# Kernel optimization log

Measured on AMD Instinct MI355X. Metric: run time of the kernel, lower is better.

The kernel has to match this reference:

```python
import jax, jax.numpy as jnp
import numpy as np

DIM = 512
NH, NKV, HD = 8, 4, DIM // 8
KVD = NKV * HD
EPS = 1.1920928955078125e-07  # torch.finfo(float32).eps (F.rms_norm default)
ROPE_BASE = 10000.0


def _rms_norm(x):
    # F.rms_norm over last dim, no learned weight
    ms = jnp.mean(jnp.square(x), axis=-1, keepdims=True)
    return x * jax.lax.rsqrt(ms + EPS)


def _rope_tables(T, dtype):
    inv_freq = 1.0 / (ROPE_BASE ** (jnp.arange(0, HD, 2, dtype=jnp.float32) / HD))
    t = jnp.arange(T, dtype=jnp.float32)
    f = jnp.outer(t, inv_freq)  # [T, HD//2]
    return jnp.cos(f).astype(dtype)[None, None], jnp.sin(f).astype(dtype)[None, None]


def _apply_rot(x, c, s):
    h = x.shape[-1] // 2
    x1, x2 = x[..., :h], x[..., h:]
    return jnp.concatenate((x1 * c + x2 * s, -x1 * s + x2 * c), axis=-1)


def setup_inputs() -> dict:
    key = jax.random.key(0)
    ks = jax.random.split(key, 5)
    B, T = 8, 2048
    x = jax.random.normal(ks[0], (B, T, DIM), dtype=jnp.float32)
    # torch Linear weights: [out_features, in_features]
    Wq = jax.random.normal(ks[1], (DIM, DIM), dtype=jnp.float32) * (DIM ** -0.5)
    Wk = jax.random.normal(ks[2], (KVD, DIM), dtype=jnp.float32) * (DIM ** -0.5)
    Wv = jax.random.normal(ks[3], (KVD, DIM), dtype=jnp.float32) * (DIM ** -0.5)
    Wp = jax.random.normal(ks[4], (DIM, DIM), dtype=jnp.float32) * (DIM ** -0.5)
    return {"x": x, "Wq": Wq, "Wk": Wk, "Wv": Wv, "Wp": Wp}


def reference(x, Wq, Wk, Wv, Wp):
    B, T, C = x.shape
    q = (x @ Wq.T).reshape(B, T, NH, HD).transpose(0, 2, 1, 3)    # [B,NH,T,HD]
    k = (x @ Wk.T).reshape(B, T, NKV, HD).transpose(0, 2, 1, 3)   # [B,NKV,T,HD]
    v = (x @ Wv.T).reshape(B, T, NKV, HD).transpose(0, 2, 1, 3)
    q, k = _rms_norm(q), _rms_norm(k)
    c, s = _rope_tables(T, q.dtype)
    q, k = _apply_rot(q, c, s), _apply_rot(k, c, s)
    rep = NH // NKV
    k = jnp.repeat(k, rep, axis=1)  # GQA expand -> [B,NH,T,HD]
    v = jnp.repeat(v, rep, axis=1)
    scale = 1.0 / jnp.sqrt(jnp.asarray(HD, dtype=q.dtype))
    scores = jnp.einsum('bhqd,bhkd->bhqk', q, k) * scale
    causal = jnp.tril(jnp.ones((T, T), dtype=bool))
    scores = jnp.where(causal[None, None], scores, jnp.finfo(scores.dtype).min)
    attn = jax.nn.softmax(scores, axis=-1)
    y = jnp.einsum('bhqk,bhkd->bhqd', attn, v)
    y = y.transpose(0, 2, 1, 3).reshape(B, T, C)
    return y @ Wp.T
```

## Files before the change

kernel.cpp:

```cpp
#include <hip/hip_runtime.h>
#include <hip/hip_bf16.h>
#include <stdint.h>

typedef __bf16 bf16;
typedef __bf16 bf16x8 __attribute__((ext_vector_type(8)));
typedef __bf16 bf16x4 __attribute__((ext_vector_type(4)));
typedef float f32x4 __attribute__((ext_vector_type(4)));

#define T_SEQ 2048
#define DIM_ 512
#define NH_ 8
#define NKV_ 4
#define HD_ 64
#define BT_ (8 * T_SEQ)
#define NEG_INF (-1e30f)
#define EPS_ 1.1920928955078125e-07f
#define QSCALE 0.18033688011112042f
#define SMAX 12.0f

#define OFF_XB   (size_t)(0)
#define OFF_WQKV (size_t)(16777216)
#define OFF_WP   (size_t)(17825792)
#define OFF_COS  (size_t)(18350080)
#define OFF_SIN  (size_t)(18612224)
#define OFF_QT   (size_t)(18874368)
#define OFF_KT   (size_t)(35651584)
#define OFF_VT   (size_t)(44040192)
#define OFF_Y    (size_t)(52428800)
#define WS_NEEDED (size_t)(69206016)

__device__ inline void mfma16(f32x4& acc, bf16x8 a, bf16x8 b) {
    acc = __builtin_amdgcn_mfma_f32_16x16x32_bf16(a, b, acc, 0, 0, 0);
}

typedef const __attribute__((address_space(1))) uint8_t* gas_ptr;
typedef __attribute__((address_space(3))) uint8_t* las_ptr;
__device__ inline void gload16(const bf16* g, bf16* l) {
    __builtin_amdgcn_global_load_lds((gas_ptr)(const void*)g, (las_ptr)(void*)l, 16, 0, 0);
}

__device__ inline bf16x4 cvt4(const float4& a) {
    bf16x4 v;
    v[0] = (bf16)a.x; v[1] = (bf16)a.y; v[2] = (bf16)a.z; v[3] = (bf16)a.w;
    return v;
}

__global__ void prep_kernel(const float* __restrict__ x, const float* __restrict__ wq,
                            const float* __restrict__ wk, const float* __restrict__ wv,
                            const float* __restrict__ wp,
                            bf16* __restrict__ xb, bf16* __restrict__ wqkv,
                            bf16* __restrict__ wpb, float* __restrict__ cosT,
                            float* __restrict__ sinT) {
    int tid = blockIdx.x * blockDim.x + threadIdx.x;
    int stride = gridDim.x * blockDim.x;
    for (int i = tid; i < BT_ * DIM_ / 4; i += stride)
        *(bf16x4*)(xb + (size_t)i * 4) = cvt4(((const float4*)x)[i]);
    for (int i = tid; i < 1024 * 512 / 4; i += stride) {
        int e = i * 4;
        int j = e >> 9, k = e & 511;
        const float* src;
        if (j < 512) src = wq + (size_t)j * 512 + k;
        else if (j < 768) src = wk + (size_t)(j - 512) * 512 + k;
        else src = wv + (size_t)(j - 768) * 512 + k;
        *(bf16x4*)(wqkv + (size_t)e) = cvt4(*(const float4*)src);
    }
    for (int i = tid; i < 512 * 512 / 4; i += stride)
        *(bf16x4*)(wpb + (size_t)i * 4) = cvt4(((const float4*)wp)[i]);
    for (int i = tid; i < T_SEQ * 32; i += stride) {
        int t = i >> 5, d = i & 31;
        float inv = powf(10000.0f, -(float)d * (1.0f / 32.0f));
        float f = (float)t * inv;
        cosT[i] = cosf(f);
        sinT[i] = sinf(f);
    }
}

__global__ __launch_bounds__(256) void qkv_gemm(const bf16* __restrict__ A,
                                                const bf16* __restrict__ B,
                                                bf16* __restrict__ qt,
                                                bf16* __restrict__ kt,
                                                bf16* __restrict__ vt,
                                                const float* __restrict__ cosT,
                                                const float* __restrict__ sinT) {
    __shared__ __align__(16) char smem[34816];
    bf16* As = (bf16*)smem;
    bf16* Bs = (bf16*)(smem + 16384);
    const int tid = threadIdx.x, lane = tid & 63, wid = tid >> 6;
    const int wr = wid >> 1, wc = wid & 1;
    const int lm = lane & 15, hi = lane >> 4;
    const int bid = blockIdx.x;
    const int swz = (bid & 7) * 128 + (bid >> 3);
    const int brow = (swz & 127) * 128;
    const int bcol = (swz >> 7) * 128;

    f32x4 acc[4][4] = {};
    for (int k0 = 0; k0 < 512; k0 += 64) {
        __syncthreads();
#pragma unroll
        for (int i = 0; i < 4; ++i) {
            int c = i * 256 + tid;
            int slot = c >> 6, l = c & 63;
            int row = (slot >> 1) * 16 + (l & 15);
            int kc = (slot & 1) * 32 + (l >> 4) * 8;
            gload16(A + (size_t)(brow + row) * 512 + k0 + kc, As + c * 8);
            gload16(B + (size_t)(bcol + row) * 512 + k0 + kc, Bs + c * 8);
        }
        asm volatile("s_waitcnt vmcnt(0)" ::: "memory");
        __syncthreads();
#pragma unroll
        for (int kk = 0; kk < 2; ++kk) {
            bf16x8 af[4], bfr[4];
#pragma unroll
            for (int m = 0; m < 4; ++m)
                af[m] = *(const bf16x8*)(As + (((wr * 4 + m) * 2 + kk) * 64 + lane) * 8);
#pragma unroll
            for (int n = 0; n < 4; ++n)
                bfr[n] = *(const bf16x8*)(Bs + (((wc * 4 + n) * 2 + kk) * 64 + lane) * 8);
            __builtin_amdgcn_s_setprio(1);
#pragma unroll
            for (int m = 0; m < 4; ++m)
#pragma unroll
                for (int n = 0; n < 4; ++n) mfma16(acc[m][n], af[m], bfr[n]);
            __builtin_amdgcn_s_setprio(0);
        }
    }
    __syncthreads();

    bf16* Tb = (bf16*)smem + wid * 4224;
    const int wcol = bcol + wc * 64;
    const int ctype = (wcol < 512) ? 0 : (wcol < 768 ? 1 : 2);

    if (ctype < 2) {
#pragma unroll
        for (int m = 0; m < 4; ++m)
#pragma unroll
            for (int r = 0; r < 4; ++r) {
                float v0 = acc[m][0][r], v1 = acc[m][1][r];
                float v2 = acc[m][2][r], v3 = acc[m][3][r];
                float ss = v0 * v0 + v1 * v1 + v2 * v2 + v3 * v3;
                ss += __shfl_xor(ss, 1);
                ss += __shfl_xor(ss, 2);
                ss += __shfl_xor(ss, 4);
                ss += __shfl_xor(ss, 8);
                float rinv = rsqrtf(ss * (1.0f / 64.0f) + EPS_);
                v0 *= rinv; v1 *= rinv; v2 *= rinv; v3 *= rinv;
                int rl = m * 16 + hi * 4 + r;
                int t = (brow + wr * 64 + rl) & (T_SEQ - 1);
                float c0 = cosT[t * 32 + lm], s0 = sinT[t * 32 + lm];
                float c1 = cosT[t * 32 + 16 + lm], s1 = sinT[t * 32 + 16 + lm];
                float o0 = v0 * c0 + v2 * s0;
                float o2 = v2 * c0 - v0 * s0;
                float o1 = v1 * c1 + v3 * s1;
                float o3 = v3 * c1 - v1 * s1;
                if (ctype == 0) { o0 *= QSCALE; o1 *= QSCALE; o2 *= QSCALE; o3 *= QSCALE; }
                Tb[rl * 66 + lm]      = (bf16)o0;
                Tb[rl * 66 + 16 + lm] = (bf16)o1;
                Tb[rl * 66 + 32 + lm] = (bf16)o2;
                Tb[rl * 66 + 48 + lm] = (bf16)o3;
            }
    } else {
#pragma unroll
        for (int m = 0; m < 4; ++m)
#pragma unroll
            for (int n = 0; n < 4; ++n)
#pragma unroll
                for (int r = 0; r < 4; ++r)
                    Tb[(n * 16 + lm) * 66 + m * 16 + hi * 4 + r] = (bf16)acc[m][n][r];
    }
    __syncthreads();

    const int i0 = brow + wr * 64;
    const int b = i0 >> 11, tt = i0 & (T_SEQ - 1);
#pragma unroll
    for (int p = 0; p < 8; ++p) {
        int row = p * 8 + (lane >> 3);
        int ch = lane & 7;
        bf16x8 val = *(const bf16x8*)(Tb + row * 66 + ch * 8);
        if (ctype == 0) {
            int head = wcol >> 6;
            *(bf16x8*)(qt + ((size_t)((b << 3) + head) * T_SEQ + tt + row) * 64 + ch * 8) = val;
        } else if (ctype == 1) {
            int head = (wcol - 512) >> 6;
            *(bf16x8*)(kt + ((size_t)((b << 2) + head) * T_SEQ + tt + row) * 64 + ch * 8) = val;
        } else {
            int head = (wcol - 768) >> 6;
            *(bf16x8*)(vt + ((size_t)((b << 2) + head) * 64 + row) * T_SEQ + tt + ch * 8) = val;
        }
    }
}

__global__ __launch_bounds__(512, 4) void attn_kernel(const bf16* __restrict__ qt,
                                                      const bf16* __restrict__ kt,
                                                      const bf16* __restrict__ vt,
                                                      bf16* __restrict__ y) {
    __shared__ bf16 Klds[4096];
    __shared__ bf16 Vlds[4096];
    __shared__ bf16 Plds[8][1152];
    const int tid = threadIdx.x;
    const int lane = tid & 63, wid = tid >> 6;
    const int lm = lane & 15, hi = lane >> 4;
    const int bid = blockIdx.x;
    const int s4 = bid >> 8;
    const int g4 = (bid >> 6) & 3;
    const int bh = bid & 63;
    const int p = 4 * (3 - s4) + ((g4 + s4) & 3);
    const int b = bh >> 3, h = bh & 7, hv = h >> 1;
    const bf16* Q = qt + (size_t)bh * T_SEQ * HD_;
    const bf16* K = kt + (size_t)(b * NKV_ + hv) * T_SEQ * HD_;
    const bf16* V = vt + (size_t)(b * NKV_ + hv) * HD_ * T_SEQ;
    const int qB = p * 128;
    const int qw = qB + wid * 16;
    bf16* Pl = &Plds[wid][0];

    const int sl0 = tid >> 6, l0 = tid & 63;
    const int gr0 = (sl0 >> 1) * 16 + (l0 & 15);
    const int gc0 = (sl0 & 1) * 32 + (l0 >> 4) * 8;
    const bf16* kg0 = K + (size_t)gr0 * HD_ + gc0;
    const bf16* vg0 = V + (size_t)gr0 * T_SEQ + gc0;
    bf16* kd0 = Klds + (size_t)tid * 8;
    bf16* vd0 = Vlds + (size_t)tid * 8;

    bf16x8 qf[2];
#pragma unroll
    for (int kk = 0; kk < 2; ++kk)
        qf[kk] = *(const bf16x8*)(Q + (size_t)(qw + lm) * HD_ + 32 * kk + 8 * hi);

    bf16x8 vones;
#pragma unroll
    for (int j = 0; j < 8; ++j) vones[j] = (bf16)1.0f;

    f32x4 o[4] = {};
    f32x4 lacc = {};

    const int nt = (qB >> 6) + 2;
    for (int t = 0; t < nt; ++t) {
        const int kv0 = t << 6;
        __syncthreads();
        {
            size_t ko = (size_t)kv0 * HD_, vo = (size_t)kv0;
            gload16(kg0 + ko, kd0);
            gload16(vg0 + vo, vd0);
        }
        asm volatile("s_waitcnt vmcnt(0)" ::: "memory");
        __syncthreads();

        if (kv0 <= qw + 15) {
            f32x4 s[4] = {};
#pragma unroll
            for (int kk = 0; kk < 2; ++kk) {
                bf16x8 kf[4];
#pragma unroll
                for (int n = 0; n < 4; ++n)
                    kf[n] = *(const bf16x8*)(Klds + ((n * 2 + kk) * 64 + lane) * 8);
#pragma unroll
                for (int n = 0; n < 4; ++n) mfma16(s[n], kf[n], qf[kk]);
            }
            const bool partial = (kv0 + 63 > qw);
            const int qg = qw + lm;
            bf16x4 pw[4];
#pragma unroll
            for (int n = 0; n < 4; ++n)
#pragma unroll
                for (int r = 0; r < 4; ++r) {
                    float xv = s[n][r];
                    if (partial)
                        xv = ((kv0 + 16 * n + 4 * hi + r) <= qg) ? xv : NEG_INF;
                    pw[n][r] = (bf16)__builtin_amdgcn_exp2f(xv - SMAX);
                }
#pragma unroll
            for (int kk = 0; kk < 2; ++kk) {
                *(bf16x4*)(Pl + lm * 40 + 4 * hi)      = pw[2 * kk];
                *(bf16x4*)(Pl + lm * 40 + 16 + 4 * hi) = pw[2 * kk + 1];
                bf16x8 vf[4], pf;
                pf = *(const bf16x8*)(Pl + lm * 40 + 8 * hi);
#pragma unroll
                for (int nd = 0; nd < 4; ++nd)
                    vf[nd] = *(const bf16x8*)(Vlds + ((nd * 2 + kk) * 64 + lane) * 8);
#pragma unroll
                for (int nd = 0; nd < 4; ++nd) mfma16(o[nd], vf[nd], pf);
                mfma16(lacc, vones, pf);
            }
        }
    }

    float rcl = 1.0f / lacc[0];
#pragma unroll
    for (int nd = 0; nd < 4; ++nd) {
        bf16x4 ov;
#pragma unroll
        for (int r = 0; r < 4; ++r) ov[r] = (bf16)(o[nd][r] * rcl);
        *(bf16x4*)(Pl + lm * 72 + nd * 16 + 4 * hi) = ov;
    }
#pragma unroll
    for (int it = 0; it < 2; ++it) {
        int chunk = it * 64 + lane;
        int row = chunk >> 3, dc = (chunk & 7) * 8;
        bf16x8 val = *(const bf16x8*)(Pl + row * 72 + dc);
        *(bf16x8*)(y + (size_t)(b * T_SEQ + qw + row) * DIM_ + h * HD_ + dc) = val;
    }
}

__global__ __launch_bounds__(256) void proj_gemm(const bf16* __restrict__ A,
                                                 const bf16* __restrict__ B,
                                                 float* __restrict__ out) {
    __shared__ __align__(16) char smem[32768];
    bf16* As = (bf16*)smem;
    bf16* Bs = (bf16*)(smem + 16384);
    const int tid = threadIdx.x, lane = tid & 63, wid = tid >> 6;
    const int wr = wid >> 1, wc = wid & 1;
    const int lm = lane & 15, hi = lane >> 4;
    const int bid = blockIdx.x;
    const int swz = (bid & 7) * 64 + (bid >> 3);
    const int brow = (swz & 127) * 128;
    const int bcol = (swz >> 7) * 128;

    f32x4 acc[4][4] = {};
    for (int k0 = 0; k0 < 512; k0 += 64) {
        __syncthreads();
#pragma unroll
        for (int i = 0; i < 4; ++i) {
            int c = i * 256 + tid;
            int slot = c >> 6, l = c & 63;
            int row = (slot >> 1) * 16 + (l & 15);
            int kc = (slot & 1) * 32 + (l >> 4) * 8;
            gload16(A + (size_t)(brow + row) * 512 + k0 + kc, As + c * 8);
            gload16(B + (size_t)(bcol + row) * 512 + k0 + kc, Bs + c * 8);
        }
        asm volatile("s_waitcnt vmcnt(0)" ::: "memory");
        __syncthreads();
#pragma unroll
        for (int kk = 0; kk < 2; ++kk) {
            bf16x8 af[4], bfr[4];
#pragma unroll
            for (int m = 0; m < 4; ++m)
                af[m] = *(const bf16x8*)(As + (((wr * 4 + m) * 2 + kk) * 64 + lane) * 8);
#pragma unroll
            for (int n = 0; n < 4; ++n)
                bfr[n] = *(const bf16x8*)(Bs + (((wc * 4 + n) * 2 + kk) * 64 + lane) * 8);
            __builtin_amdgcn_s_setprio(1);
#pragma unroll
            for (int m = 0; m < 4; ++m)
#pragma unroll
                for (int n = 0; n < 4; ++n) mfma16(acc[m][n], af[m], bfr[n]);
            __builtin_amdgcn_s_setprio(0);
        }
    }
#pragma unroll
    for (int m = 0; m < 4; ++m)
#pragma unroll
        for (int n = 0; n < 4; ++n)
#pragma unroll
            for (int r = 0; r < 4; ++r) {
                int i = brow + wr * 64 + m * 16 + hi * 4 + r;
                int j = bcol + wc * 64 + n * 16 + lm;
                out[(size_t)i * DIM_ + j] = acc[m][n][r];
            }
}

extern "C" void kernel_launch(void* const* d_in, const int* in_sizes, int n_in,
                              void* d_out, int out_size, void* d_ws, size_t ws_size,
                              hipStream_t stream) {
    const float* x  = (const float*)d_in[0];
    const float* wq = (const float*)d_in[1];
    const float* wk = (const float*)d_in[2];
    const float* wv = (const float*)d_in[3];
    const float* wp = (const float*)d_in[4];
    if (ws_size < WS_NEEDED) return;

    char* ws = (char*)d_ws;
    bf16* xb    = (bf16*)(ws + OFF_XB);
    bf16* wqkv  = (bf16*)(ws + OFF_WQKV);
    bf16* wpb   = (bf16*)(ws + OFF_WP);
    float* cosT = (float*)(ws + OFF_COS);
    float* sinT = (float*)(ws + OFF_SIN);
    bf16* qt    = (bf16*)(ws + OFF_QT);
    bf16* kt    = (bf16*)(ws + OFF_KT);
    bf16* vt    = (bf16*)(ws + OFF_VT);
    bf16* y     = (bf16*)(ws + OFF_Y);

    prep_kernel<<<2048, 256, 0, stream>>>(x, wq, wk, wv, wp, xb, wqkv, wpb, cosT, sinT);

    qkv_gemm<<<1024, 256, 0, stream>>>(xb, wqkv, qt, kt, vt, cosT, sinT);

    attn_kernel<<<1024, 512, 0, stream>>>(qt, kt, vt, y);

    proj_gemm<<<512, 256, 0, stream>>>(y, wpb, (float*)d_out);
}
```

Before: 136.3 us.

## Double-buffer K/V tiles in LDS to overlap global loads with compute

Allocates two LDS buffers for K and V and prefetches the next KV tile while the current tile's QK and PV MFMAs run. A partial vmcnt wait replaces the full drain, and raw barriers replace __syncthreads. This hides global-to-LDS load latency behind compute, at the cost of doubling K/V LDS usage, which may reduce blocks per CU.

```diff
diff --git a/kernel.cpp b/kernel.cpp
--- a/kernel.cpp
+++ b/kernel.cpp
@@ -193,8 +193,8 @@
                                                       const bf16* __restrict__ kt,
                                                       const bf16* __restrict__ vt,
                                                       bf16* __restrict__ y) {
-    __shared__ bf16 Klds[4096];
-    __shared__ bf16 Vlds[4096];
+    __shared__ bf16 Klds[2][4096];
+    __shared__ bf16 Vlds[2][4096];
     __shared__ bf16 Plds[8][1152];
     const int tid = threadIdx.x;
     const int lane = tid & 63, wid = tid >> 6;
@@ -217,8 +217,16 @@
     const int gc0 = (sl0 & 1) * 32 + (l0 >> 4) * 8;
     const bf16* kg0 = K + (size_t)gr0 * HD_ + gc0;
     const bf16* vg0 = V + (size_t)gr0 * T_SEQ + gc0;
-    bf16* kd0 = Klds + (size_t)tid * 8;
-    bf16* vd0 = Vlds + (size_t)tid * 8;
+    bf16* kd0 = &Klds[0][0] + (size_t)tid * 8;
+    bf16* vd0 = &Vlds[0][0] + (size_t)tid * 8;
+
+#define STAGE_KV(t, buf) do {                                \
+        size_t ko = (size_t)(t) * (64 * HD_);                \
+        size_t vo = (size_t)(t) * 64;                        \
+        size_t bo = (size_t)(buf) * 4096;                    \
+        gload16(kg0 + ko, kd0 + bo);                         \
+        gload16(vg0 + vo, vd0 + bo);                         \
+    } while (0)
 
     bf16x8 qf[2];
 #pragma unroll
@@ -233,25 +241,28 @@
     f32x4 lacc = {};
 
     const int nt = (qB >> 6) + 2;
+    STAGE_KV(0, 0);
     for (int t = 0; t < nt; ++t) {
         const int kv0 = t << 6;
-        __syncthreads();
-        {
-            size_t ko = (size_t)kv0 * HD_, vo = (size_t)kv0;
-            gload16(kg0 + ko, kd0);
-            gload16(vg0 + vo, vd0);
-        }
-        asm volatile("s_waitcnt vmcnt(0)" ::: "memory");
-        __syncthreads();
+        const int cur = t & 1;
+        if (t + 1 < nt) {
+            STAGE_KV(t + 1, cur ^ 1);
+            asm volatile("s_waitcnt vmcnt(2)" ::: "memory");
+        } else {
+            asm volatile("s_waitcnt vmcnt(0)" ::: "memory");
+        }
+        __builtin_amdgcn_s_barrier();
 
         if (kv0 <= qw + 15) {
+            const bf16* Kb = &Klds[cur][0];
+            const bf16* Vb = &Vlds[cur][0];
             f32x4 s[4] = {};
 #pragma unroll
             for (int kk = 0; kk < 2; ++kk) {
                 bf16x8 kf[4];
 #pragma unroll
                 for (int n = 0; n < 4; ++n)
-                    kf[n] = *(const bf16x8*)(Klds + ((n * 2 + kk) * 64 + lane) * 8);
+                    kf[n] = *(const bf16x8*)(Kb + ((n * 2 + kk) * 64 + lane) * 8);
 #pragma unroll
                 for (int n = 0; n < 4; ++n) mfma16(s[n], kf[n], qf[kk]);
             }
@@ -275,13 +286,15 @@
                 pf = *(const bf16x8*)(Pl + lm * 40 + 8 * hi);
 #pragma unroll
                 for (int nd = 0; nd < 4; ++nd)
-                    vf[nd] = *(const bf16x8*)(Vlds + ((nd * 2 + kk) * 64 + lane) * 8);
+                    vf[nd] = *(const bf16x8*)(Vb + ((nd * 2 + kk) * 64 + lane) * 8);
 #pragma unroll
                 for (int nd = 0; nd < 4; ++nd) mfma16(o[nd], vf[nd], pf);
                 mfma16(lacc, vones, pf);
             }
         }
-    }
+        __builtin_amdgcn_s_barrier();
+    }
+#undef STAGE_KV
 
     float rcl = 1.0f / lacc[0];
 #pragma unroll
```

Result: slower. 143.3 us (+5.1%).
